# Optimization experiments

Hardware: AMD Instinct MI355X
Metric: run time of the kernel (lower is better)

Reference implementation:

```python
import jax, jax.numpy as jnp
import numpy as np

B, LF, RATE = 2, 2048, 4
DF, DS, H = 1024, 1024, 8
D2 = DF // 2            # 512: both self (d1) and cross (d2) branch dims (equal split)
POOL_H = 2048
TS = LF // RATE         # 512 slow steps


def _p(key, shape):
    return jax.random.normal(key, shape, jnp.float32) * 0.02


def setup_inputs() -> dict:
    keys = iter(jax.random.split(jax.random.key(0), 32))
    inp = {
        "x_fast": jax.random.normal(next(keys), (B, LF, DF), jnp.float32),
        "x_slow": jax.random.normal(next(keys), (B, TS, DS), jnp.float32),
    }
    for name in ("fself", "fcross", "sself", "scross"):
        inp[f"{name}_wqkv"] = _p(next(keys), (D2, 3 * D2))
        inp[f"{name}_bqkv"] = jnp.zeros((3 * D2,), jnp.float32)
        inp[f"{name}_wo"] = _p(next(keys), (D2, D2))
        inp[f"{name}_bo"] = jnp.zeros((D2,), jnp.float32)
    inp["lift_w"] = _p(next(keys), (DS, D2))
    inp["lift_b"] = jnp.zeros((D2,), jnp.float32)
    inp["pool_w1"] = _p(next(keys), (RATE * DF, POOL_H))
    inp["pool_b1"] = jnp.zeros((POOL_H,), jnp.float32)
    inp["pool_w2"] = _p(next(keys), (POOL_H, D2))
    inp["pool_b2"] = jnp.zeros((D2,), jnp.float32)
    return inp


def _mha(q_in, k_in, v_in, wqkv, bqkv, wo, bo):
    """Standard multihead attention with fused in-proj weight [d, 3d]."""
    b, tq, d = q_in.shape
    hd = d // H
    q = q_in @ wqkv[:, :d] + bqkv[:d]
    k = k_in @ wqkv[:, d:2 * d] + bqkv[d:2 * d]
    v = v_in @ wqkv[:, 2 * d:] + bqkv[2 * d:]
    q = q.reshape(b, tq, H, hd)
    k = k.reshape(b, k_in.shape[1], H, hd)
    v = v.reshape(b, v_in.shape[1], H, hd)
    scores = jnp.einsum('bqhd,bkhd->bhqk', q, k) * np.float32(1.0 / np.sqrt(hd))
    w = jax.nn.softmax(scores, axis=-1)
    o = jnp.einsum('bhqk,bkhd->bqhd', w, v).reshape(b, tq, d)
    return o @ wo + bo


def _forward(x_fast, x_slow,
             fself_wqkv, fself_bqkv, fself_wo, fself_bo,
             fcross_wqkv, fcross_bqkv, fcross_wo, fcross_bo,
             sself_wqkv, sself_bqkv, sself_wo, sself_bo,
             scross_wqkv, scross_bqkv, scross_wo, scross_bo,
             lift_w, lift_b, pool_w1, pool_b1, pool_w2, pool_b2):
    b = x_fast.shape[0]
    # ---- fast level: lift slow -> fast timescale (ffn applied before repeat)
    y = jnp.repeat(x_slow @ lift_w + lift_b, RATE, axis=1)          # [B, LF, D2]
    x1, x2 = x_fast[..., :D2], x_fast[..., D2:]
    z_fast = jnp.concatenate([
        _mha(x1, x1, x1, fself_wqkv, fself_bqkv, fself_wo, fself_bo),
        _mha(x2, y, y, fcross_wqkv, fcross_bqkv, fcross_wo, fcross_bo),
    ], axis=-1)
    # ---- slow level: causal block pooling of fast sequence
    blocks = x_fast.reshape(b, TS, RATE * DF)                        # LF == TS*RATE
    s = jax.nn.gelu(blocks @ pool_w1 + pool_b1) @ pool_w2 + pool_b2  # [B, TS, D2]
    # causal shift: prepend zero slow step, drop last (zero in pooled feature dim)
    s = jnp.concatenate([jnp.zeros((b, 1, D2), s.dtype), s[:, :-1]], axis=1)
    s1, s2 = x_slow[..., :D2], x_slow[..., D2:]
    z_slow = jnp.concatenate([
        _mha(s1, s1, s1, sself_wqkv, sself_bqkv, sself_wo, sself_bo),
        _mha(s2, s, s, scross_wqkv, scross_bqkv, scross_wo, scross_bo),
    ], axis=-1)
    return z_fast, z_slow


def reference(x_fast, x_slow,
              fself_wqkv, fself_bqkv, fself_wo, fself_bo,
              fcross_wqkv, fcross_bqkv, fcross_wo, fcross_bo,
              sself_wqkv, sself_bqkv, sself_wo, sself_bo,
              scross_wqkv, scross_bqkv, scross_wo, scross_bo,
              lift_w, lift_b, pool_w1, pool_b1, pool_w2, pool_b2):
    return _forward(x_fast, x_slow,
                    fself_wqkv, fself_bqkv, fself_wo, fself_bo,
                    fcross_wqkv, fcross_bqkv, fcross_wo, fcross_bo,
                    sself_wqkv, sself_bqkv, sself_wo, sself_bo,
                    scross_wqkv, scross_bqkv, scross_wo, scross_bo,
                    lift_w, lift_b, pool_w1, pool_b1, pool_w2, pool_b2)
```

## Files before the change

kernel.cpp:

```cpp
#include <hip/hip_runtime.h>
#include <hip/hip_bf16.h>


typedef __attribute__((ext_vector_type(8))) short bf16x8;
typedef __attribute__((ext_vector_type(4))) float f32x4;
typedef unsigned short u16;
typedef unsigned int u32;

__device__ inline u16 f2bf(float f) {
    __hip_bfloat16 h = __float2bfloat16(f);
    return *reinterpret_cast<u16*>(&h);
}
__device__ inline u32 pack2(float a, float b) {
    return (u32)f2bf(a) | ((u32)f2bf(b) << 16);
}
__device__ inline float bf2f(u16 h) {
    u32 x = ((u32)h) << 16; float f;
    __builtin_memcpy(&f, &x, 4);
    return f;
}
__device__ inline void gld16(const u16* g, u16* l) {
    __builtin_amdgcn_global_load_lds(
        (const __attribute__((address_space(1))) void*)(g),
        (__attribute__((address_space(3))) void*)(l), 16, 0, 0);
}
template <int N>
__device__ inline void wait_vmcnt() {
    if constexpr (N == 0)      asm volatile("s_waitcnt vmcnt(0)" ::: "memory");
    else if constexpr (N == 4) asm volatile("s_waitcnt vmcnt(4)" ::: "memory");
    else if constexpr (N == 8) asm volatile("s_waitcnt vmcnt(8)" ::: "memory");
}

struct GDesc {
    const u16* A; const u16* Bt; const float* bias;
    void* out0; u16* aux0; u16* aux1;
    int lda, ldb, ldc, K, ntx, mode, rshift, tile_end;
};
struct GPack { int n; int pad[3]; GDesc d[8]; };

struct ADesc { const u16* Q; const u16* K; const u16* Vt; u16* O; int Rq, nk, tile_end, q0b; };
struct APack { int n; int pad[3]; ADesc d[2]; };

struct WDesc { const float* src; u16* dst; int ldn, K, tx_, tile_end; };
struct WPack { int n; int pad[3]; WDesc d[12]; };

struct CvtA { const float* a; u16* da; int na8; const float* b; u16* db; };
struct GeluA { u16* p0; const u16* p1; const float* bias; };

template <int TMT>
__device__ __forceinline__ void gemm_body(const GPack& pk, int bid, u16* smem)
{
    constexpr int TM = TMT * 16;
    constexpr int W = TMT / 2;
    constexpr int BUF = TM * 64;
    constexpr int NLD = TM / 32 * 2;
    u16* As = smem;
    u16* Bs = smem + 2 * BUF;

    int di = 0;
    while (bid >= pk.d[di].tile_end) ++di;
    const GDesc g = pk.d[di];
    const int base = di ? pk.d[di - 1].tile_end : 0;
    const int local = bid - base;

    const int total = g.tile_end - base;
    const int tpx = total >> 3;
    const int T = (local & 7) * tpx + (local >> 3);
    const int tx = (T >> 2) % g.ntx;
    const int ty = ((T / (g.ntx << 2)) << 2) + (T & 3);
    const int row0 = ty * TM, col0 = tx * TM;

    const int t = threadIdx.x;
    const int wave = t >> 6, lane = t & 63;
    const int l15 = lane & 15, quad = lane >> 4;
    const int wm = (wave >> 1) * W * 16, wn = (wave & 1) * W * 16;

    const int srow = wave * 8 + (lane >> 3);
    const int ssw = (((lane & 7) ^ (lane >> 3))) * 8;
    const u16* Ag = g.A + (long long)(row0 + srow) * g.lda + ssw;
    const u16* Bg = g.Bt + (long long)(col0 + srow) * g.ldb + ssw;

    const int c0 = (quad ^ (l15 & 7)) * 8;

    f32x4 acc[W][W];
#pragma unroll
    for (int i = 0; i < W; ++i)
#pragma unroll
        for (int j = 0; j < W; ++j) {
            acc[i][j][0] = 0.f; acc[i][j][1] = 0.f;
            acc[i][j][2] = 0.f; acc[i][j][3] = 0.f;
        }

    auto stage = [&](int buf, int k0) {
#pragma unroll
        for (int r = 0; r < TM / 32; ++r) {
            gld16(Ag + (long long)r * 32 * g.lda + k0, As + buf * BUF + r * 2048 + wave * 512);
            gld16(Bg + (long long)r * 32 * g.ldb + k0, Bs + buf * BUF + r * 2048 + wave * 512);
        }
    };
    auto compute = [&](int buf) {
        const u16* Ab = As + buf * BUF;
        const u16* Bb = Bs + buf * BUF;
#pragma unroll
        for (int kc = 0; kc < 2; ++kc) {
            const int cc = kc ? (c0 ^ 32) : c0;
            bf16x8 af[W], bfr[W];
#pragma unroll
            for (int i = 0; i < W; ++i) {
                af[i]  = *(const bf16x8*)(Ab + (wm + i * 16 + l15) * 64 + cc);
                bfr[i] = *(const bf16x8*)(Bb + (wn + i * 16 + l15) * 64 + cc);
            }
#pragma unroll
            for (int i = 0; i < W; ++i)
#pragma unroll
                for (int j = 0; j < W; ++j)
                    acc[i][j] = __builtin_amdgcn_mfma_f32_16x16x32_bf16(af[i], bfr[j], acc[i][j], 0, 0, 0);
        }
    };

    const int nt = g.K >> 6;
    stage(0, 0);
    for (int tt = 0; tt < nt; ++tt) {
        const int cur = tt & 1;
        if (tt + 1 < nt) {
            stage(cur ^ 1, (tt + 1) << 6);
            wait_vmcnt<NLD>();
        } else {
            wait_vmcnt<0>();
        }
        __builtin_amdgcn_sched_barrier(0);
        __builtin_amdgcn_s_barrier();
        __builtin_amdgcn_sched_barrier(0);
        compute(cur);
        __builtin_amdgcn_sched_barrier(0);
        __builtin_amdgcn_s_barrier();
    }

    const int rmask = (1 << g.rshift) - 1;
#pragma unroll
    for (int i = 0; i < W; ++i)
#pragma unroll
        for (int j = 0; j < W; ++j)
#pragma unroll
            for (int r = 0; r < 4; ++r) {
                int m = row0 + wm + i * 16 + quad * 4 + r;
                int n = col0 + wn + j * 16 + l15;
                float v = acc[i][j][r];
                if (g.mode != 5) v += g.bias[n];
                if (g.mode == 0) {
                    ((float*)g.out0)[(long long)m * g.ldc + n] = v;
                } else if (g.mode == 1 || g.mode == 5) {
                    ((u16*)g.out0)[(long long)m * g.ldc + n] = f2bf(v);
                } else if (g.mode == 2) {
                    float x3 = v * v * v;
                    v = 0.5f * v * (1.f + tanhf(0.7978845608028654f * (v + 0.044715f * x3)));
                    ((u16*)g.out0)[(long long)m * g.ldc + n] = f2bf(v);
                } else if (g.mode == 3) {
                    u16 h = f2bf(v);
                    if (n < 512) ((u16*)g.out0)[(long long)m * 512 + n] = h;
                    else if (n < 1024) g.aux0[(long long)m * 512 + (n - 512)] = h;
                    else {
                        int d = n - 1024;
                        int bb = m >> g.rshift, rr = m & rmask;
                        g.aux1[((long long)((bb * 8 + (d >> 6)) * 64 + (d & 63)) << g.rshift) + rr] = h;
                    }
                } else if (g.mode == 4) {
                    u16 h = f2bf(v);
                    if (n < 512) ((u16*)g.out0)[(long long)m * 512 + n] = h;
                    else {
                        int d = n - 512;
                        int bb = m >> g.rshift, rr = m & rmask;
                        g.aux1[((long long)((bb * 8 + (d >> 6)) * 64 + (d & 63)) << g.rshift) + rr] = h;
                    }
                } else {
                    int t9 = m & 511;
                    if (t9 != 511) ((u16*)g.out0)[(long long)(m + 1) * g.ldc + n] = f2bf(v);
                    if (t9 == 0)  ((u16*)g.out0)[(long long)m * g.ldc + n] = 0;
                }
            }
}

#define ALD 72

__device__ __forceinline__ void attn_body(const APack& pk, int bid, u16* smem, float prescale)
{
    u16* Qs  = smem;
    u16* Ks  = smem + 4096;
    u16* Vts = smem + 12288;
    u16* Psb = smem + 20480;

    int di = 0;
    while (bid >= pk.d[di].tile_end) ++di;
    const ADesc g = pk.d[di];
    const int base = di ? pk.d[di - 1].tile_end : 0;
    const int local = bid - base;

    const int t = threadIdx.x;
    const int wave = t >> 6, lane = t & 63;
    const int l15 = lane & 15, quad = lane >> 4;
    const int bh = local & 15, b = bh >> 3, h = bh & 7;
    const int q0 = g.q0b + (local >> 4) * 64;
    const int nk = g.nk;

    const int srow = wave * 8 + (lane >> 3);
    const int ssw = (((lane & 7) ^ (lane >> 3))) * 8;
    const int c0 = (quad ^ (l15 & 7)) * 8;

    const u16* Qg = g.Q + ((long long)(b * g.Rq + q0 + srow) << 9) + h * 64 + ssw;
    const u16* Kg = g.K + ((long long)(b * nk + srow) << 9) + h * 64 + ssw;
    const u16* Vg = g.Vt + (long long)bh * 64 * nk + (long long)srow * nk + ssw;

    auto stage = [&](int buf, int kt) {
#pragma unroll
        for (int r = 0; r < 2; ++r) {
            gld16(Kg + ((long long)(kt + r * 32) << 9), Ks + buf * 4096 + r * 2048 + wave * 512);
            gld16(Vg + (long long)r * 32 * nk + kt, Vts + buf * 4096 + r * 2048 + wave * 512);
        }
    };

#pragma unroll
    for (int r = 0; r < 2; ++r)
        gld16(Qg + ((long long)r * 32 << 9), Qs + r * 2048 + wave * 512);
    stage(0, 0);
    wait_vmcnt<4>();
    __builtin_amdgcn_sched_barrier(0);
    __builtin_amdgcn_s_barrier();
    __builtin_amdgcn_sched_barrier(0);

    bf16x8 qf[2];
    qf[0] = *(const bf16x8*)(Qs + (wave * 16 + l15) * 64 + c0);
    qf[1] = *(const bf16x8*)(Qs + (wave * 16 + l15) * 64 + (c0 ^ 32));

    f32x4 Oacc[4];
#pragma unroll
    for (int nt2 = 0; nt2 < 4; ++nt2) { Oacc[nt2][0] = 0.f; Oacc[nt2][1] = 0.f; Oacc[nt2][2] = 0.f; Oacc[nt2][3] = 0.f; }
    float lr[4] = {0.f, 0.f, 0.f, 0.f};

    u16* Pw = Psb + wave * 16 * ALD;

    auto acompute = [&](int buf) {
        const u16* Kb = Ks + buf * 4096;
        const u16* Vb = Vts + buf * 4096;
#pragma unroll
        for (int k16 = 0; k16 < 4; ++k16) {
            f32x4 s;
            s[0] = 0.f; s[1] = 0.f; s[2] = 0.f; s[3] = 0.f;
            bf16x8 kf0 = *(const bf16x8*)(Kb + (k16 * 16 + l15) * 64 + c0);
            bf16x8 kf1 = *(const bf16x8*)(Kb + (k16 * 16 + l15) * 64 + (c0 ^ 32));
            __builtin_amdgcn_s_setprio(1);
            s = __builtin_amdgcn_mfma_f32_16x16x32_bf16(qf[0], kf0, s, 0, 0, 0);
            s = __builtin_amdgcn_mfma_f32_16x16x32_bf16(qf[1], kf1, s, 0, 0, 0);
            __builtin_amdgcn_s_setprio(0);
#pragma unroll
            for (int r = 0; r < 4; ++r) {
                float p = exp2f(s[r] * prescale);
                lr[r] += p;
                Pw[(quad * 4 + r) * ALD + k16 * 16 + l15] = f2bf(p);
            }
        }
        bf16x8 pf0 = *(const bf16x8*)(Pw + l15 * ALD + quad * 8);
        bf16x8 pf1 = *(const bf16x8*)(Pw + l15 * ALD + 32 + quad * 8);
        __builtin_amdgcn_s_setprio(1);
#pragma unroll
        for (int nt2 = 0; nt2 < 4; ++nt2) {
            bf16x8 vf0 = *(const bf16x8*)(Vb + (nt2 * 16 + l15) * 64 + c0);
            bf16x8 vf1 = *(const bf16x8*)(Vb + (nt2 * 16 + l15) * 64 + (c0 ^ 32));
            Oacc[nt2] = __builtin_amdgcn_mfma_f32_16x16x32_bf16(pf0, vf0, Oacc[nt2], 0, 0, 0);
            Oacc[nt2] = __builtin_amdgcn_mfma_f32_16x16x32_bf16(pf1, vf1, Oacc[nt2], 0, 0, 0);
        }
        __builtin_amdgcn_s_setprio(0);
    };

    const int nt = nk >> 6;
    for (int tt = 0; tt < nt; ++tt) {
        const int cur = tt & 1;
        if (tt + 1 < nt) {
            stage(cur ^ 1, (tt + 1) << 6);
            wait_vmcnt<4>();
        } else {
            wait_vmcnt<0>();
        }
        __builtin_amdgcn_sched_barrier(0);
        __builtin_amdgcn_s_barrier();
        __builtin_amdgcn_sched_barrier(0);
        acompute(cur);
        __builtin_amdgcn_sched_barrier(0);
        __builtin_amdgcn_s_barrier();
    }

    float inv[4];
#pragma unroll
    for (int r = 0; r < 4; ++r) {
        float s = lr[r];
#pragma unroll
        for (int off = 1; off < 16; off <<= 1) s += __shfl_xor(s, off);
        inv[r] = 1.f / s;
    }

    u16* Ob = g.O + ((long long)(b * g.Rq + q0 + wave * 16 + quad * 4) << 9) + h * 64;
#pragma unroll
    for (int nt2 = 0; nt2 < 4; ++nt2)
#pragma unroll
        for (int r = 0; r < 4; ++r)
            Ob[(long long)r * 512 + nt2 * 16 + l15] = f2bf(Oacc[nt2][r] * inv[r]);
}

__device__ __forceinline__ void wt_body(const WPack& pk, int bid, u16* smem)
{
    float* T = (float*)smem;
    int di = 0;
    while (bid >= pk.d[di].tile_end) ++di;
    const WDesc g = pk.d[di];
    const int base = di ? pk.d[di - 1].tile_end : 0;
    const int local = bid - base;
    const int k0 = (local % g.tx_) * 64;
    const int n0 = (local / g.tx_) * 64;
    const int t = threadIdx.x;
#pragma unroll
    for (int i = 0; i < 4; ++i) {
        int idx = t + i * 256;
        int r = idx >> 4, c4 = idx & 15;
        float4 v = *(const float4*)(g.src + (long long)(k0 + r) * g.ldn + n0 + c4 * 4);
        T[r * 68 + c4 * 4 + 0] = v.x; T[r * 68 + c4 * 4 + 1] = v.y;
        T[r * 68 + c4 * 4 + 2] = v.z; T[r * 68 + c4 * 4 + 3] = v.w;
    }
    __syncthreads();
#pragma unroll
    for (int i = 0; i < 4; ++i) {
        int idx = t + i * 256;
        int rn = idx >> 4, k4 = idx & 15;
        uint2 u;
        u.x = pack2(T[(k4 * 4 + 0) * 68 + rn], T[(k4 * 4 + 1) * 68 + rn]);
        u.y = pack2(T[(k4 * 4 + 2) * 68 + rn], T[(k4 * 4 + 3) * 68 + rn]);
        *(uint2*)(g.dst + (long long)(n0 + rn) * g.K + k0 + k4 * 4) = u;
    }
}

__device__ __forceinline__ void cvt_body(const CvtA& cv, int bid)
{
    int i = bid * 256 + threadIdx.x;
    const float* s; u16* d;
    if (i < cv.na8) { s = cv.a + (long long)i * 8; d = cv.da + (long long)i * 8; }
    else { s = cv.b + (long long)(i - cv.na8) * 8; d = cv.db + (long long)(i - cv.na8) * 8; }
    float4 x = *(const float4*)s;
    float4 y = *(const float4*)(s + 4);
    uint4 u;
    u.x = pack2(x.x, x.y); u.y = pack2(x.z, x.w);
    u.z = pack2(y.x, y.y); u.w = pack2(y.z, y.w);
    *(uint4*)d = u;
}

__device__ __forceinline__ void gelu_body(const GeluA& ge, int bid)
{
    int i8 = (bid * 256 + threadIdx.x) * 8;
    uint4 a = *(const uint4*)(ge.p0 + i8);
    uint4 b = *(const uint4*)(ge.p1 + i8);
    int n = i8 & 2047;
    float4 bi0 = *(const float4*)(ge.bias + n);
    float4 bi1 = *(const float4*)(ge.bias + n + 4);
    float bb[8] = {bi0.x, bi0.y, bi0.z, bi0.w, bi1.x, bi1.y, bi1.z, bi1.w};
    u32 aw[4] = {a.x, a.y, a.z, a.w};
    u32 bw[4] = {b.x, b.y, b.z, b.w};
    u32 ow[4];
#pragma unroll
    for (int k = 0; k < 4; ++k) {
        float v0 = bf2f((u16)(aw[k] & 0xffff)) + bf2f((u16)(bw[k] & 0xffff)) + bb[2 * k];
        float v1 = bf2f((u16)(aw[k] >> 16)) + bf2f((u16)(bw[k] >> 16)) + bb[2 * k + 1];
        float x3 = v0 * v0 * v0;
        v0 = 0.5f * v0 * (1.f + tanhf(0.7978845608028654f * (v0 + 0.044715f * x3)));
        x3 = v1 * v1 * v1;
        v1 = 0.5f * v1 * (1.f + tanhf(0.7978845608028654f * (v1 + 0.044715f * x3)));
        ow[k] = pack2(v0, v1);
    }
    uint4 o; o.x = ow[0]; o.y = ow[1]; o.z = ow[2]; o.w = ow[3];
    *(uint4*)(ge.p0 + i8) = o;
}

template <int TMT>
__global__ __launch_bounds__(256)
void fat_multi(APack ap, GPack gp, WPack wp, GeluA ge, CvtA cv,
               int na, int ngm, int nwt, int ncv, float prescale)
{
    constexpr int GB = 2 * 2 * (TMT * 16 * 64) * 2;
    constexpr int SB = (GB > 50176) ? GB : 50176;
    __shared__ __align__(16) u16 smem[SB / 2];
    int bid = blockIdx.x;
    if (bid < na) { attn_body(ap, bid, smem, prescale); return; }
    bid -= na;
    if (bid < ngm) { gemm_body<TMT>(gp, bid, smem); return; }
    bid -= ngm;
    if (bid < nwt) { wt_body(wp, bid, smem); return; }
    bid -= nwt;
    if (bid < ncv) { cvt_body(cv, bid); return; }
    gelu_body(ge, bid - ncv);
}

extern "C" void kernel_launch(void* const* d_in, const int* in_sizes, int n_in,
                              void* d_out, int out_size, void* d_ws, size_t ws_size,
                              hipStream_t stream)
{
    const float* x_fast      = (const float*)d_in[0];
    const float* x_slow      = (const float*)d_in[1];
    const float* fself_wqkv  = (const float*)d_in[2];
    const float* fself_bqkv  = (const float*)d_in[3];
    const float* fself_wo    = (const float*)d_in[4];
    const float* fself_bo    = (const float*)d_in[5];
    const float* fcross_wqkv = (const float*)d_in[6];
    const float* fcross_bqkv = (const float*)d_in[7];
    const float* fcross_wo   = (const float*)d_in[8];
    const float* fcross_bo   = (const float*)d_in[9];
    const float* sself_wqkv  = (const float*)d_in[10];
    const float* sself_bqkv  = (const float*)d_in[11];
    const float* sself_wo    = (const float*)d_in[12];
    const float* sself_bo    = (const float*)d_in[13];
    const float* scross_wqkv = (const float*)d_in[14];
    const float* scross_bqkv = (const float*)d_in[15];
    const float* scross_wo   = (const float*)d_in[16];
    const float* scross_bo   = (const float*)d_in[17];
    const float* lift_w      = (const float*)d_in[18];
    const float* lift_b      = (const float*)d_in[19];
    const float* pool_w1     = (const float*)d_in[20];
    const float* pool_b1     = (const float*)d_in[21];
    const float* pool_w2     = (const float*)d_in[22];
    const float* pool_b2     = (const float*)d_in[23];

    float* out = (float*)d_out;
    float* zf = out;
    float* zs = out + 2LL * 2048 * 1024;

    float* ws = (float*)d_ws;
    u16* pw1T     = (u16*)(ws + 0);
    u16* wqkvT_f  = (u16*)(ws + 4194304);
    u16* wqkvT_c  = (u16*)(ws + 4587520);
    u16* wqkvT_s  = (u16*)(ws + 4980736);
    u16* wqkvT_sc = (u16*)(ws + 5373952);
    u16* liftT    = (u16*)(ws + 5767168);
    u16* pw2T     = (u16*)(ws + 6029312);
    u16* woT_f    = (u16*)(ws + 6553600);
    u16* woT_c    = (u16*)(ws + 6684672);
    u16* woT_s    = (u16*)(ws + 6815744);
    u16* woT_sc   = (u16*)(ws + 6946816);
    u16* xfb      = (u16*)(ws + 7077888);
    u16* xsb      = (u16*)(ws + 9175040);
    u16* q1       = (u16*)(ws + 9699328);
    u16* k1       = (u16*)(ws + 10747904);
    u16* vt1      = (u16*)(ws + 11796480);
    u16* qs       = (u16*)(ws + 12845056);
    u16* ks       = (u16*)(ws + 13107200);
    u16* vts      = (u16*)(ws + 13369344);
    u16* qcs      = (u16*)(ws + 13631488);
    u16* k2    = (u16*)(ws + 0);
    u16* vt2   = (u16*)(ws + 262144);
    u16* sbufS = (u16*)(ws + 524288);
    u16* kcs   = (u16*)(ws + 786432);
    u16* vtcs  = (u16*)(ws + 1048576);
    u16* fo1   = (u16*)(ws + 1310720);
    u16* fo2   = (u16*)(ws + 2359296);
    u16* so1   = (u16*)(ws + 3407872);
    u16* so2   = (u16*)(ws + 3670016);
    u16* q2   = (u16*)(out + 0);
    u16* ybuf = (u16*)(out + 1048576);
    u16* hbuf = (u16*)(out + 1310720);
    u16* p1b  = (u16*)(out + 2359296);

    const float PRESCALE = 0.125f * 1.4426950408889634f;
    APack a_null{}; GPack g_null{}; WPack w_null{}; GeluA ge_null{}; CvtA cv_null{};

    auto gl = [&](GPack& p, int i, const u16* A, int lda,
                  const u16* Bt, int ldb, const float* bias,
                  void* out0, int ldc, int M, int N, int K, int mode,
                  u16* aux0, u16* aux1, int rshift, int TM, int& te) {
        te += (M / TM) * (N / TM);
        p.d[i] = GDesc{A, Bt, bias, out0, aux0, aux1,
                       lda, ldb, ldc, K, N / TM, mode, rshift, te};
    };

    {
        WPack wp; wp.n = 11; int te = 0, i = 0;
        auto add = [&](const float* s, u16* d, int ldn, int K, int N) {
            te += (K / 64) * (N / 64);
            wp.d[i++] = WDesc{s, d, ldn, K, K / 64, te};
        };
        add(pool_w1, pw1T, 2048, 4096, 2048);
        add(fself_wqkv, wqkvT_f, 1536, 512, 1536);
        add(fcross_wqkv, wqkvT_c, 1536, 512, 1536);
        add(sself_wqkv, wqkvT_s, 1536, 512, 1536);
        add(scross_wqkv, wqkvT_sc, 1536, 512, 1536);
        add(lift_w, liftT, 512, 1024, 512);
        add(pool_w2, pw2T, 512, 2048, 512);
        add(fself_wo, woT_f, 512, 512, 512);
        add(fcross_wo, woT_c, 512, 512, 512);
        add(sself_wo, woT_s, 512, 512, 512);
        add(scross_wo, woT_sc, 512, 512, 512);
        CvtA cv{x_fast, xfb, 524288, x_slow, xsb};
        hipLaunchKernelGGL(fat_multi<4>, dim3(te + 2560), dim3(256), 0, stream,
                           a_null, g_null, wp, ge_null, cv, 0, 0, te, 2560, PRESCALE);
    }

    {
        GPack p; p.n = 7; int te = 0;
        gl(p, 0, xfb, 4096, pw1T, 4096, pool_b1, hbuf, 2048,
           1024, 2048, 2048, 5, 0, 0, 0, 128, te);
        gl(p, 1, xfb + 2048, 4096, pw1T + 2048, 4096, pool_b1, p1b, 2048,
           1024, 2048, 2048, 5, 0, 0, 0, 128, te);
        gl(p, 2, xfb, 1024, wqkvT_f, 512, fself_bqkv, q1, 512,
           4096, 1536, 512, 3, k1, vt1, 11, 128, te);
        gl(p, 3, xfb + 512, 1024, wqkvT_c, 512, fcross_bqkv, q2, 512,
           4096, 512, 512, 1, 0, 0, 0, 128, te);
        gl(p, 4, xsb, 1024, wqkvT_s, 512, sself_bqkv, qs, 512,
           1024, 1536, 512, 3, ks, vts, 9, 128, te);
        gl(p, 5, xsb, 1024, liftT, 1024, lift_b, ybuf, 512,
           1024, 512, 1024, 1, 0, 0, 0, 128, te);
        gl(p, 6, xsb + 512, 1024, wqkvT_sc, 512, scross_bqkv, qcs, 512,
           1024, 512, 512, 1, 0, 0, 0, 128, te);
        hipLaunchKernelGGL(fat_multi<8>, dim3(te), dim3(256), 0, stream,
                           a_null, p, w_null, ge_null, cv_null, 0, te, 0, 0, PRESCALE);
    }

    {
        APack ap; ap.n = 2;
        ap.d[0] = ADesc{q1, k1, vt1, fo1, 2048, 2048, 256, 0};
        ap.d[1] = ADesc{qs, ks, vts, so1, 512, 512, 384, 0};
        GeluA ge{hbuf, p1b, pool_b1};
        hipLaunchKernelGGL(fat_multi<4>, dim3(384 + 1024), dim3(256), 0, stream,
                           ap, g_null, w_null, ge, cv_null, 384, 0, 0, 0, PRESCALE);
    }

    {
        APack ap; ap.n = 1;
        ap.d[0] = ADesc{q1, k1, vt1, fo1, 2048, 2048, 256, 1024};
        GPack p; p.n = 2; int te = 0;
        gl(p, 0, ybuf, 512, wqkvT_c + 512 * 512, 512, fcross_bqkv + 512, k2, 512,
           1024, 1024, 512, 4, 0, vt2, 9, 64, te);
        gl(p, 1, hbuf, 2048, pw2T, 2048, pool_b2, sbufS, 512,
           1024, 512, 2048, 6, 0, 0, 0, 64, te);
        hipLaunchKernelGGL(fat_multi<4>, dim3(256 + te), dim3(256), 0, stream,
                           ap, p, w_null, ge_null, cv_null, 256, te, 0, 0, PRESCALE);
    }

    {
        APack ap; ap.n = 1;
        ap.d[0] = ADesc{q2, k2, vt2, fo2, 2048, 512, 512, 0};
        GPack p; p.n = 1; int te = 0;
        gl(p, 0, sbufS, 512, wqkvT_sc + 512 * 512, 512, scross_bqkv + 512, kcs, 512,
           1024, 1024, 512, 4, 0, vtcs, 9, 64, te);
        hipLaunchKernelGGL(fat_multi<4>, dim3(512 + te), dim3(256), 0, stream,
                           ap, p, w_null, ge_null, cv_null, 512, te, 0, 0, PRESCALE);
    }

    {
        APack ap; ap.n = 1;
        ap.d[0] = ADesc{qcs, kcs, vtcs, so2, 512, 512, 128, 0};
        GPack p; p.n = 3; int te = 0;
        gl(p, 0, fo1, 512, woT_f, 512, fself_bo, zf, 1024,
           4096, 512, 512, 0, 0, 0, 0, 64, te);
        gl(p, 1, fo2, 512, woT_c, 512, fcross_bo, zf + 512, 1024,
           4096, 512, 512, 0, 0, 0, 0, 64, te);
        gl(p, 2, so1, 512, woT_s, 512, sself_bo, zs, 1024,
           1024, 512, 512, 0, 0, 0, 0, 64, te);
        hipLaunchKernelGGL(fat_multi<4>, dim3(128 + te), dim3(256), 0, stream,
                           ap, p, w_null, ge_null, cv_null, 128, te, 0, 0, PRESCALE);
    }

    {
        GPack p; p.n = 1; int te = 0;
        gl(p, 0, so2, 512, woT_sc, 512, scross_bo, zs + 512, 1024,
           1024, 512, 512, 0, 0, 0, 0, 64, te);
        hipLaunchKernelGGL(fat_multi<4>, dim3(te), dim3(256), 0, stream,
                           a_null, p, w_null, ge_null, cv_null, 0, te, 0, 0, PRESCALE);
    }
}
```

Measured before the change: 350.4 us.

## Run pool GEMM with full K and fused GELU, merge attention launches

The first pool projection previously ran as two K-split halves followed by a separate GELU pass that summed them. It now runs as one GEMM over the full K=4096 using mode 2, which presumably applies bias and GELU in the epilogue, so the separate GELU blocks and the partial buffer go away. The pool-w2 and lift K/V GEMMs move earlier, into the launch that runs the first attention stage. The second fast-self attention half and the fast-cross attention now share one launch, which removes a kernel launch. The trade-off is fewer, longer-K GEMM tiles in the big launch, which reduces parallelism for that projection, and a changed dependency schedule that must remain correct.

```diff
diff --git a/kernel.cpp b/kernel.cpp
--- a/kernel.cpp
+++ b/kernel.cpp
@@ -45,7 +45,6 @@
 struct WPack { int n; int pad[3]; WDesc d[12]; };
 
 struct CvtA { const float* a; u16* da; int na8; const float* b; u16* db; };
-struct GeluA { u16* p0; const u16* p1; const float* bias; };
 
 template <int TMT>
 __device__ __forceinline__ void gemm_body(const GPack& pk, int bid, u16* smem)
@@ -350,36 +349,10 @@
     *(uint4*)d = u;
 }
 
-__device__ __forceinline__ void gelu_body(const GeluA& ge, int bid)
-{
-    int i8 = (bid * 256 + threadIdx.x) * 8;
-    uint4 a = *(const uint4*)(ge.p0 + i8);
-    uint4 b = *(const uint4*)(ge.p1 + i8);
-    int n = i8 & 2047;
-    float4 bi0 = *(const float4*)(ge.bias + n);
-    float4 bi1 = *(const float4*)(ge.bias + n + 4);
-    float bb[8] = {bi0.x, bi0.y, bi0.z, bi0.w, bi1.x, bi1.y, bi1.z, bi1.w};
-    u32 aw[4] = {a.x, a.y, a.z, a.w};
-    u32 bw[4] = {b.x, b.y, b.z, b.w};
-    u32 ow[4];
-#pragma unroll
-    for (int k = 0; k < 4; ++k) {
-        float v0 = bf2f((u16)(aw[k] & 0xffff)) + bf2f((u16)(bw[k] & 0xffff)) + bb[2 * k];
-        float v1 = bf2f((u16)(aw[k] >> 16)) + bf2f((u16)(bw[k] >> 16)) + bb[2 * k + 1];
-        float x3 = v0 * v0 * v0;
-        v0 = 0.5f * v0 * (1.f + tanhf(0.7978845608028654f * (v0 + 0.044715f * x3)));
-        x3 = v1 * v1 * v1;
-        v1 = 0.5f * v1 * (1.f + tanhf(0.7978845608028654f * (v1 + 0.044715f * x3)));
-        ow[k] = pack2(v0, v1);
-    }
-    uint4 o; o.x = ow[0]; o.y = ow[1]; o.z = ow[2]; o.w = ow[3];
-    *(uint4*)(ge.p0 + i8) = o;
-}
-
 template <int TMT>
 __global__ __launch_bounds__(256)
-void fat_multi(APack ap, GPack gp, WPack wp, GeluA ge, CvtA cv,
-               int na, int ngm, int nwt, int ncv, float prescale)
+void fat_multi(APack ap, GPack gp, WPack wp, CvtA cv,
+               int na, int ngm, int nwt, float prescale)
 {
     constexpr int GB = 2 * 2 * (TMT * 16 * 64) * 2;
     constexpr int SB = (GB > 50176) ? GB : 50176;
@@ -390,9 +363,7 @@
     if (bid < ngm) { gemm_body<TMT>(gp, bid, smem); return; }
     bid -= ngm;
     if (bid < nwt) { wt_body(wp, bid, smem); return; }
-    bid -= nwt;
-    if (bid < ncv) { cvt_body(cv, bid); return; }
-    gelu_body(ge, bid - ncv);
+    cvt_body(cv, bid - nwt);
 }
 
 extern "C" void kernel_launch(void* const* d_in, const int* in_sizes, int n_in,
@@ -461,10 +432,9 @@
     u16* q2   = (u16*)(out + 0);
     u16* ybuf = (u16*)(out + 1048576);
     u16* hbuf = (u16*)(out + 1310720);
-    u16* p1b  = (u16*)(out + 2359296);
 
     const float PRESCALE = 0.125f * 1.4426950408889634f;
-    APack a_null{}; GPack g_null{}; WPack w_null{}; GeluA ge_null{}; CvtA cv_null{};
+    APack a_null{}; GPack g_null{}; WPack w_null{}; CvtA cv_null{};
 
     auto gl = [&](GPack& p, int i, const u16* A, int lda,
                   const u16* Bt, int ldb, const float* bias,
@@ -494,58 +464,49 @@
         add(scross_wo, woT_sc, 512, 512, 512);
         CvtA cv{x_fast, xfb, 524288, x_slow, xsb};
         hipLaunchKernelGGL(fat_multi<4>, dim3(te + 2560), dim3(256), 0, stream,
-                           a_null, g_null, wp, ge_null, cv, 0, 0, te, 2560, PRESCALE);
+                           a_null, g_null, wp, cv, 0, 0, te, PRESCALE);
     }
 
     {
-        GPack p; p.n = 7; int te = 0;
+        GPack p; p.n = 6; int te = 0;
         gl(p, 0, xfb, 4096, pw1T, 4096, pool_b1, hbuf, 2048,
-           1024, 2048, 2048, 5, 0, 0, 0, 128, te);
-        gl(p, 1, xfb + 2048, 4096, pw1T + 2048, 4096, pool_b1, p1b, 2048,
-           1024, 2048, 2048, 5, 0, 0, 0, 128, te);
-        gl(p, 2, xfb, 1024, wqkvT_f, 512, fself_bqkv, q1, 512,
+           1024, 2048, 4096, 2, 0, 0, 0, 128, te);
+        gl(p, 1, xfb, 1024, wqkvT_f, 512, fself_bqkv, q1, 512,
            4096, 1536, 512, 3, k1, vt1, 11, 128, te);
-        gl(p, 3, xfb + 512, 1024, wqkvT_c, 512, fcross_bqkv, q2, 512,
+        gl(p, 2, xfb + 512, 1024, wqkvT_c, 512, fcross_bqkv, q2, 512,
            4096, 512, 512, 1, 0, 0, 0, 128, te);
-        gl(p, 4, xsb, 1024, wqkvT_s, 512, sself_bqkv, qs, 512,
+        gl(p, 3, xsb, 1024, wqkvT_s, 512, sself_bqkv, qs, 512,
            1024, 1536, 512, 3, ks, vts, 9, 128, te);
-        gl(p, 5, xsb, 1024, liftT, 1024, lift_b, ybuf, 512,
+        gl(p, 4, xsb, 1024, liftT, 1024, lift_b, ybuf, 512,
            1024, 512, 1024, 1, 0, 0, 0, 128, te);
-        gl(p, 6, xsb + 512, 1024, wqkvT_sc, 512, scross_bqkv, qcs, 512,
+        gl(p, 5, xsb + 512, 1024, wqkvT_sc, 512, scross_bqkv, qcs, 512,
            1024, 512, 512, 1, 0, 0, 0, 128, te);
         hipLaunchKernelGGL(fat_multi<8>, dim3(te), dim3(256), 0, stream,
-                           a_null, p, w_null, ge_null, cv_null, 0, te, 0, 0, PRESCALE);
+                           a_null, p, w_null, cv_null, 0, te, 0, PRESCALE);
     }
 
     {
         APack ap; ap.n = 2;
         ap.d[0] = ADesc{q1, k1, vt1, fo1, 2048, 2048, 256, 0};
         ap.d[1] = ADesc{qs, ks, vts, so1, 512, 512, 384, 0};
-        GeluA ge{hbuf, p1b, pool_b1};
-        hipLaunchKernelGGL(fat_multi<4>, dim3(384 + 1024), dim3(256), 0, stream,
-                           ap, g_null, w_null, ge, cv_null, 384, 0, 0, 0, PRESCALE);
+        GPack p; p.n = 2; int te = 0;
+        gl(p, 0, hbuf, 2048, pw2T, 2048, pool_b2, sbufS, 512,
+           1024, 512, 2048, 6, 0, 0, 0, 64, te);
+        gl(p, 1, ybuf, 512, wqkvT_c + 512 * 512, 512, fcross_bqkv + 512, k2, 512,
+           1024, 1024, 512, 4, 0, vt2, 9, 64, te);
+        hipLaunchKernelGGL(fat_multi<4>, dim3(384 + te), dim3(256), 0, stream,
+                           ap, p, w_null, cv_null, 384, te, 0, PRESCALE);
     }
 
     {
-        APack ap; ap.n = 1;
+        APack ap; ap.n = 2;
         ap.d[0] = ADesc{q1, k1, vt1, fo1, 2048, 2048, 256, 1024};
-        GPack p; p.n = 2; int te = 0;
-        gl(p, 0, ybuf, 512, wqkvT_c + 512 * 512, 512, fcross_bqkv + 512, k2, 512,
-           1024, 1024, 512, 4, 0, vt2, 9, 64, te);
-        gl(p, 1, hbuf, 2048, pw2T, 2048, pool_b2, sbufS, 512,
-           1024, 512, 2048, 6, 0, 0, 0, 64, te);
-        hipLaunchKernelGGL(fat_multi<4>, dim3(256 + te), dim3(256), 0, stream,
-                           ap, p, w_null, ge_null, cv_null, 256, te, 0, 0, PRESCALE);
-    }
-
-    {
-        APack ap; ap.n = 1;
-        ap.d[0] = ADesc{q2, k2, vt2, fo2, 2048, 512, 512, 0};
+        ap.d[1] = ADesc{q2, k2, vt2, fo2, 2048, 512, 768, 0};
         GPack p; p.n = 1; int te = 0;
         gl(p, 0, sbufS, 512, wqkvT_sc + 512 * 512, 512, scross_bqkv + 512, kcs, 512,
            1024, 1024, 512, 4, 0, vtcs, 9, 64, te);
-        hipLaunchKernelGGL(fat_multi<4>, dim3(512 + te), dim3(256), 0, stream,
-                           ap, p, w_null, ge_null, cv_null, 512, te, 0, 0, PRESCALE);
+        hipLaunchKernelGGL(fat_multi<4>, dim3(768 + te), dim3(256), 0, stream,
+                           ap, p, w_null, cv_null, 768, te, 0, PRESCALE);
     }
 
     {
@@ -559,7 +520,7 @@
         gl(p, 2, so1, 512, woT_s, 512, sself_bo, zs, 1024,
            1024, 512, 512, 0, 0, 0, 0, 64, te);
         hipLaunchKernelGGL(fat_multi<4>, dim3(128 + te), dim3(256), 0, stream,
-                           ap, p, w_null, ge_null, cv_null, 128, te, 0, 0, PRESCALE);
+                           ap, p, w_null, cv_null, 128, te, 0, PRESCALE);
     }
 
     {
@@ -567,6 +528,6 @@
         gl(p, 0, so2, 512, woT_sc, 512, scross_bo, zs + 512, 1024,
            1024, 512, 512, 0, 0, 0, 0, 64, te);
         hipLaunchKernelGGL(fat_multi<4>, dim3(te), dim3(256), 0, stream,
-                           a_null, p, w_null, ge_null, cv_null, 0, te, 0, 0, PRESCALE);
-    }
-}
+                           a_null, p, w_null, cv_null, 0, te, 0, PRESCALE);
+    }
+}
```

Measured after the change: 332.8 us (median of 2 runs). -5.0%, faster.
